# Optimization experiments

Hardware: AMD Instinct MI355X
Metric: run time of the kernel (lower is better)

Reference implementation:

```python
import jax, jax.numpy as jnp
import numpy as np

N_NODES = 100000
N_EDGES = 1600000
IN_DIM, HID_DIM, OUT_DIM = 32, 16, 8


def setup_inputs() -> dict:
    key = jax.random.key(0)
    ks = jax.random.split(key, 10)
    x = jax.random.normal(ks[0], (N_NODES, IN_DIM), dtype=jnp.float32)
    edge_index = jax.random.randint(ks[1], (2, N_EDGES), 0, N_NODES, dtype=jnp.int32)
    s1 = 1.0 / np.sqrt(IN_DIM)
    s2 = 1.0 / np.sqrt(HID_DIM)
    s3 = 1.0 / np.sqrt(OUT_DIM)
    return {
        "x": x,
        "edge_index": edge_index,
        # SAGEConv layer 1: lin_l (neighbor, with bias) and lin_r (root)
        "Wl1": jax.random.uniform(ks[2], (HID_DIM, IN_DIM), jnp.float32, -s1, s1),
        "bl1": jnp.zeros((HID_DIM,), jnp.float32),
        "Wr1": jax.random.uniform(ks[3], (HID_DIM, IN_DIM), jnp.float32, -s1, s1),
        # SAGEConv layer 2
        "Wl2": jax.random.uniform(ks[4], (OUT_DIM, HID_DIM), jnp.float32, -s2, s2),
        "bl2": jnp.zeros((OUT_DIM,), jnp.float32),
        "Wr2": jax.random.uniform(ks[5], (OUT_DIM, HID_DIM), jnp.float32, -s2, s2),
        # final Linear head
        "Wfc": jax.random.uniform(ks[6], (1, OUT_DIM), jnp.float32, -s3, s3),
        "bfc": jax.random.uniform(ks[7], (1,), jnp.float32, -s3, s3),
    }


def _sage_conv(x, src, dst, Wl, bl, Wr):
    # mean-aggregate neighbor messages x[src] at destination nodes
    msg_sum = jax.ops.segment_sum(x[src], dst, num_segments=N_NODES)  # [N, d]
    deg = jax.ops.segment_sum(jnp.ones((src.shape[0],), x.dtype), dst, num_segments=N_NODES)
    mean = msg_sum / jnp.maximum(deg, 1.0)[:, None]
    # out = lin_l(mean_neighbors) + lin_r(x_root)
    return mean @ Wl.T + bl + x @ Wr.T


def reference(x, edge_index, Wl1, bl1, Wr1, Wl2, bl2, Wr2, Wfc, bfc):
    src, dst = edge_index[0], edge_index[1]
    h = _sage_conv(x, src, dst, Wl1, bl1, Wr1)
    h = jax.nn.relu(h)
    h = _sage_conv(h, src, dst, Wl2, bl2, Wr2)
    return h @ Wfc.T + bfc  # [N, 1]
```

## Files before the change

### kernel.cpp

```cpp
#include <hip/hip_runtime.h>
#include <hip/hip_fp16.h>

#define NN 100000
#define NE 1600000
#define IN_DIM 32
#define HID_DIM 16
#define OUT_DIM 8

#define NPB 128
#define NBK ((NN + NPB - 1) / NPB)
#define CAP 3200
#define EPB 4096
#define EPT (EPB / 256)
#define NT_BUCKET ((NE + EPB - 1) / EPB)
#define NT_PRE1 ((NN + 255) / 256)
#define GRID1 (NT_BUCKET + NT_PRE1)
#define BF_STRIDE 16
#define SCAN_CHUNKS ((NBK + 255) / 256)

__global__ __launch_bounds__(256) void k_phase1(
    const float* __restrict__ x, const int* __restrict__ src, const int* __restrict__ dst,
    const float* __restrict__ Wl1, const float* __restrict__ bl1, const float* __restrict__ Wr1,
    const float* __restrict__ Wl2, const float* __restrict__ bl2, const float* __restrict__ Wr2,
    const float* __restrict__ Wfc, const float* __restrict__ bfc,
    int* __restrict__ bucketfill, unsigned int* __restrict__ bucket,
    __half* __restrict__ zh, float* __restrict__ rb, float* __restrict__ uvc)
{
    __shared__ int lcnt[NBK];
    __shared__ int lpos[NBK];
    __shared__ int lbase[NBK];
    __shared__ int lfill[NBK];
    __shared__ int sscan[256];
    __shared__ unsigned int ssorted[EPB];
    __shared__ unsigned short sbin[EPB];
    int tid = threadIdx.x;

    if (blockIdx.x < NT_BUCKET) {
        int e0 = blockIdx.x * EPB;
        int e1 = min(e0 + EPB, NE);
        int total = e1 - e0;

        for (int i = tid; i < NBK; i += 256) lcnt[i] = 0;
        __syncthreads();

        int myd[EPT];
#pragma unroll
        for (int k = 0; k < EPT; k++) {
            int e = e0 + k * 256 + tid;
            myd[k] = (e < e1) ? dst[e] : -1;
            if (myd[k] >= 0) atomicAdd(&lcnt[myd[k] >> 7], 1);
        }
        __syncthreads();

        int carry = 0;
        for (int ch = 0; ch < SCAN_CHUNKS; ch++) {
            int idx = ch * 256 + tid;
            int v = (idx < NBK) ? lcnt[idx] : 0;
            sscan[tid] = v;
            __syncthreads();
            for (int off = 1; off < 256; off <<= 1) {
                int t2 = (tid >= off) ? sscan[tid - off] : 0;
                __syncthreads();
                sscan[tid] += t2;
                __syncthreads();
            }
            if (idx < NBK) lpos[idx] = carry + sscan[tid] - v;
            carry += sscan[255];
            __syncthreads();
        }

        for (int i = tid; i < NBK; i += 256) {
            lbase[i] = (lcnt[i] > 0) ? atomicAdd(&bucketfill[i * BF_STRIDE], lcnt[i]) : 0;
            lfill[i] = lpos[i];
        }
        __syncthreads();

#pragma unroll
        for (int k = 0; k < EPT; k++) {
            if (myd[k] >= 0) {
                int e = e0 + k * 256 + tid;
                int s = src[e];
                int b = myd[k] >> 7;
                int p = atomicAdd(&lfill[b], 1);
                ssorted[p] = (unsigned)(myd[k] & (NPB - 1)) | ((unsigned)s << 7);
                sbin[p] = (unsigned short)b;
            }
        }
        __syncthreads();

        for (int i = tid; i < total; i += 256) {
            int b = sbin[i];
            bucket[(size_t)b * CAP + lbase[b] + (i - lpos[b])] = ssorted[i];
        }
    } else {
        int chunk = blockIdx.x - NT_BUCKET;
        float* sWl = (float*)ssorted;
        float* sWr = sWl + 512;
        float* sb  = (float*)sbin;
        for (int i = tid; i < HID_DIM * IN_DIM; i += 256) {
            sWl[i] = Wl1[i];
            sWr[i] = Wr1[i];
        }
        if (tid < HID_DIM) sb[tid] = bl1[tid];
        if (chunk == 0) {
            if (tid < HID_DIM) {
                float uu = 0.f, vv = 0.f;
#pragma unroll
                for (int o = 0; o < OUT_DIM; o++) {
                    uu += Wfc[o] * Wl2[o * HID_DIM + tid];
                    vv += Wfc[o] * Wr2[o * HID_DIM + tid];
                }
                uvc[tid] = uu;
                uvc[HID_DIM + tid] = vv;
            }
            if (tid == 0) {
                float c0 = bfc[0];
#pragma unroll
                for (int o = 0; o < OUT_DIM; o++) c0 += Wfc[o] * bl2[o];
                uvc[2 * HID_DIM] = c0;
            }
        }
        __syncthreads();
        int n = chunk * 256 + tid;
        if (n < NN) {
            float xv[IN_DIM];
            const float4* x4 = (const float4*)(x + (size_t)n * IN_DIM);
#pragma unroll
            for (int c = 0; c < 8; c++) {
                float4 b = x4[c];
                xv[c * 4 + 0] = b.x; xv[c * 4 + 1] = b.y;
                xv[c * 4 + 2] = b.z; xv[c * 4 + 3] = b.w;
            }
            float zo[HID_DIM], ro[HID_DIM];
#pragma unroll
            for (int o = 0; o < HID_DIM; o++) {
                float az = 0.f, ar = sb[o];
#pragma unroll
                for (int i = 0; i < IN_DIM; i++) {
                    az += sWl[o * IN_DIM + i] * xv[i];
                    ar += sWr[o * IN_DIM + i] * xv[i];
                }
                zo[o] = az; ro[o] = ar;
            }
            __half2 hh[8];
#pragma unroll
            for (int c = 0; c < 8; c++) hh[c] = __floats2half2_rn(zo[2 * c], zo[2 * c + 1]);
            float4* zh4 = (float4*)(zh + (size_t)n * HID_DIM);
            zh4[0] = *(float4*)&hh[0];
            zh4[1] = *(float4*)&hh[4];
            float4* r4 = (float4*)(rb + (size_t)n * HID_DIM);
#pragma unroll
            for (int c = 0; c < 4; c++) {
                r4[c] = make_float4(ro[c*4], ro[c*4+1], ro[c*4+2], ro[c*4+3]);
            }
        }
    }
}

__global__ __launch_bounds__(256) void k_sort_gather(
    const int* __restrict__ bucketfill, const unsigned int* __restrict__ bucket,
    const __half* __restrict__ zh, const float* __restrict__ rb, const float* __restrict__ uvc,
    int* __restrict__ deg, float* __restrict__ sv, float* __restrict__ tv)
{
    __shared__ int lcnt[NPB];
    __shared__ int lscan[NPB];
    __shared__ int lfill[NPB];
    __shared__ int ssrc[CAP];

    int b = blockIdx.x;
    int tid = threadIdx.x;
    int cntb = bucketfill[b * BF_STRIDE];
    const unsigned int* bk = bucket + (size_t)b * CAP;

    if (tid < NPB) lcnt[tid] = 0;
    __syncthreads();
    for (int i = tid; i < cntb; i += 256) atomicAdd(&lcnt[bk[i] & (NPB - 1)], 1);
    __syncthreads();
    if (tid < NPB) lscan[tid] = lcnt[tid];
    __syncthreads();
    for (int off = 1; off < NPB; off <<= 1) {
        int tvv = (tid >= off && tid < NPB) ? lscan[tid - off] : 0;
        __syncthreads();
        if (tid < NPB) lscan[tid] += tvv;
        __syncthreads();
    }
    if (tid < NPB) {
        lfill[tid] = lscan[tid] - lcnt[tid];
        int node = b * NPB + tid;
        if (node < NN) deg[node] = lcnt[tid];
    }
    __syncthreads();
    for (int i = tid; i < cntb; i += 256) {
        unsigned v = bk[i];
        int d = v & (NPB - 1);
        int p = atomicAdd(&lfill[d], 1);
        ssrc[p] = (int)(v >> 7);
    }
    __syncthreads();

    int c = tid & 3;
    int nl0 = tid >> 2;
    float4 u4 = ((const float4*)uvc)[c];
    float4 v4 = ((const float4*)uvc)[4 + c];
    const float2* z2p = (const float2*)zh;
#pragma unroll
    for (int pass = 0; pass < 2; pass++) {
        int nl = pass * 64 + nl0;
        int n2 = b * NPB + nl;
        if (n2 < NN) {
            int dg = lcnt[nl];
            int st = lscan[nl] - dg;
            float4 acc = {0.f, 0.f, 0.f, 0.f};
            int i = 0;
            for (; i + 4 <= dg; i += 4) {
                int s0 = ssrc[st + i + 0];
                int s1 = ssrc[st + i + 1];
                int s2 = ssrc[st + i + 2];
                int s3 = ssrc[st + i + 3];
                float2 w0 = z2p[s0 * 4 + c];
                float2 w1 = z2p[s1 * 4 + c];
                float2 w2 = z2p[s2 * 4 + c];
                float2 w3 = z2p[s3 * 4 + c];
                float2 a0 = __half22float2(*(__half2*)&w0.x), b0 = __half22float2(*(__half2*)&w0.y);
                float2 a1 = __half22float2(*(__half2*)&w1.x), b1 = __half22float2(*(__half2*)&w1.y);
                float2 a2 = __half22float2(*(__half2*)&w2.x), b2 = __half22float2(*(__half2*)&w2.y);
                float2 a3 = __half22float2(*(__half2*)&w3.x), b3 = __half22float2(*(__half2*)&w3.y);
                acc.x += a0.x + a1.x + a2.x + a3.x;
                acc.y += a0.y + a1.y + a2.y + a3.y;
                acc.z += b0.x + b1.x + b2.x + b3.x;
                acc.w += b0.y + b1.y + b2.y + b3.y;
            }
            for (; i < dg; i++) {
                float2 w = z2p[ssrc[st + i] * 4 + c];
                float2 a = __half22float2(*(__half2*)&w.x), bb = __half22float2(*(__half2*)&w.y);
                acc.x += a.x; acc.y += a.y; acc.z += bb.x; acc.w += bb.y;
            }
            float inv = 1.0f / fmaxf((float)dg, 1.0f);
            float4 r = ((const float4*)rb)[n2 * 4 + c];
            float h0 = fmaxf(acc.x * inv + r.x, 0.f);
            float h1 = fmaxf(acc.y * inv + r.y, 0.f);
            float h2 = fmaxf(acc.z * inv + r.z, 0.f);
            float h3 = fmaxf(acc.w * inv + r.w, 0.f);
            float ps = u4.x * h0 + u4.y * h1 + u4.z * h2 + u4.w * h3;
            float pt = v4.x * h0 + v4.y * h1 + v4.z * h2 + v4.w * h3;
            ps += __shfl_xor(ps, 1);
            ps += __shfl_xor(ps, 2);
            pt += __shfl_xor(pt, 1);
            pt += __shfl_xor(pt, 2);
            if (c == 0) { sv[n2] = ps; tv[n2] = pt; }
        }
    }
}

__global__ __launch_bounds__(256) void k_final(
    const int* __restrict__ bucketfill, const unsigned int* __restrict__ bucket,
    const int* __restrict__ deg, const float* __restrict__ sv, const float* __restrict__ tv,
    const float* __restrict__ uvc, float* __restrict__ out)
{
    __shared__ float lsum[NPB];
    int b = blockIdx.x;
    int tid = threadIdx.x;
    int cntb = bucketfill[b * BF_STRIDE];
    const unsigned int* bk = bucket + (size_t)b * CAP;

    if (tid < NPB) lsum[tid] = 0.f;
    __syncthreads();
    for (int i = tid; i < cntb; i += 256) {
        unsigned v = bk[i];
        int d = v & (NPB - 1);
        int s = (int)(v >> 7);
        atomicAdd(&lsum[d], sv[s]);
    }
    __syncthreads();
    if (tid < NPB) {
        int n = b * NPB + tid;
        if (n < NN) {
            float dg = (float)deg[n];
            out[n] = lsum[tid] / fmaxf(dg, 1.0f) + tv[n] + uvc[2 * HID_DIM];
        }
    }
}

extern "C" void kernel_launch(void* const* d_in, const int* in_sizes, int n_in,
                              void* d_out, int out_size, void* d_ws, size_t ws_size,
                              hipStream_t stream) {
    const float* x   = (const float*)d_in[0];
    const int*   ei  = (const int*)d_in[1];
    const float* Wl1 = (const float*)d_in[2];
    const float* bl1 = (const float*)d_in[3];
    const float* Wr1 = (const float*)d_in[4];
    const float* Wl2 = (const float*)d_in[5];
    const float* bl2 = (const float*)d_in[6];
    const float* Wr2 = (const float*)d_in[7];
    const float* Wfc = (const float*)d_in[8];
    const float* bfc = (const float*)d_in[9];
    float* out = (float*)d_out;

    const int* src = ei;
    const int* dst = ei + NE;

    int* bucketfill = (int*)d_ws;
    int* deg        = bucketfill + 12544;
    float* uvc      = (float*)(deg + NN);
    float* sv       = uvc + 40;
    float* tv       = sv + NN;
    unsigned int* bucket = (unsigned int*)(tv + NN);
    __half* zh      = (__half*)(bucket + (size_t)NBK * CAP);
    float* rb       = (float*)(zh + (size_t)NN * HID_DIM);

    hipMemsetAsync(bucketfill, 0, NBK * BF_STRIDE * sizeof(int), stream);

    k_phase1<<<GRID1, 256, 0, stream>>>(x, src, dst, Wl1, bl1, Wr1,
                                        Wl2, bl2, Wr2, Wfc, bfc,
                                        bucketfill, bucket, zh, rb, uvc);
    k_sort_gather<<<NBK, 256, 0, stream>>>(bucketfill, bucket, zh, rb, uvc, deg, sv, tv);
    k_final<<<NBK, 256, 0, stream>>>(bucketfill, bucket, deg, sv, tv, uvc, out);
}
```

Baseline: 152.2 us.

## Use wavefront shuffle scans and halve edges per bucketing block

Replaces the shared-memory Hillis-Steele scans, which need many block-wide barriers, with 64-lane shuffle scans plus a small per-wave sum combine, in both the bucketing kernel and the per-bucket sort kernel. The edges handled per bucketing block drop from 4096 to 2048, which doubles the number of bucketing blocks and shrinks their shared-memory footprint. To fit the smaller ssorted buffer, the weight staging in the precompute branch moves to other shared arrays. The extra blocks each repeat the full scan over all buckets and issue more global atomics on the bucket fill counters.

```diff
diff --git a/kernel.cpp b/kernel.cpp
--- a/kernel.cpp
+++ b/kernel.cpp
@@ -10,7 +10,7 @@
 #define NPB 128
 #define NBK ((NN + NPB - 1) / NPB)
 #define CAP 3200
-#define EPB 4096
+#define EPB 2048
 #define EPT (EPB / 256)
 #define NT_BUCKET ((NE + EPB - 1) / EPB)
 #define NT_PRE1 ((NN + 255) / 256)
@@ -30,7 +30,7 @@
     __shared__ int lpos[NBK];
     __shared__ int lbase[NBK];
     __shared__ int lfill[NBK];
-    __shared__ int sscan[256];
+    __shared__ int swsum[4];
     __shared__ unsigned int ssorted[EPB];
     __shared__ unsigned short sbin[EPB];
     int tid = threadIdx.x;
@@ -39,6 +39,8 @@
         int e0 = blockIdx.x * EPB;
         int e1 = min(e0 + EPB, NE);
         int total = e1 - e0;
+        int lane = tid & 63;
+        int w = tid >> 6;
 
         for (int i = tid; i < NBK; i += 256) lcnt[i] = 0;
         __syncthreads();
@@ -56,16 +58,18 @@
         for (int ch = 0; ch < SCAN_CHUNKS; ch++) {
             int idx = ch * 256 + tid;
             int v = (idx < NBK) ? lcnt[idx] : 0;
-            sscan[tid] = v;
+            int incl = v;
+#pragma unroll
+            for (int off = 1; off < 64; off <<= 1) {
+                int t = __shfl_up(incl, off);
+                if (lane >= off) incl += t;
+            }
+            if (lane == 63) swsum[w] = incl;
             __syncthreads();
-            for (int off = 1; off < 256; off <<= 1) {
-                int t2 = (tid >= off) ? sscan[tid - off] : 0;
-                __syncthreads();
-                sscan[tid] += t2;
-                __syncthreads();
-            }
-            if (idx < NBK) lpos[idx] = carry + sscan[tid] - v;
-            carry += sscan[255];
+            int pre = carry;
+            for (int ww = 0; ww < w; ww++) pre += swsum[ww];
+            if (idx < NBK) lpos[idx] = pre + incl - v;
+            carry += swsum[0] + swsum[1] + swsum[2] + swsum[3];
             __syncthreads();
         }
 
@@ -94,9 +98,9 @@
         }
     } else {
         int chunk = blockIdx.x - NT_BUCKET;
-        float* sWl = (float*)ssorted;
-        float* sWr = sWl + 512;
-        float* sb  = (float*)sbin;
+        float* sWl = (float*)lcnt;
+        float* sWr = (float*)lbase;
+        float* sb  = (float*)ssorted;
         for (int i = tid; i < HID_DIM * IN_DIM; i += 256) {
             sWl[i] = Wl1[i];
             sWr[i] = Wr1[i];
@@ -165,6 +169,7 @@
     __shared__ int lcnt[NPB];
     __shared__ int lscan[NPB];
     __shared__ int lfill[NPB];
+    __shared__ int wsum0;
     __shared__ int ssrc[CAP];
 
     int b = blockIdx.x;
@@ -176,18 +181,25 @@
     __syncthreads();
     for (int i = tid; i < cntb; i += 256) atomicAdd(&lcnt[bk[i] & (NPB - 1)], 1);
     __syncthreads();
-    if (tid < NPB) lscan[tid] = lcnt[tid];
-    __syncthreads();
-    for (int off = 1; off < NPB; off <<= 1) {
-        int tvv = (tid >= off && tid < NPB) ? lscan[tid - off] : 0;
-        __syncthreads();
-        if (tid < NPB) lscan[tid] += tvv;
-        __syncthreads();
-    }
-    if (tid < NPB) {
-        lfill[tid] = lscan[tid] - lcnt[tid];
-        int node = b * NPB + tid;
-        if (node < NN) deg[node] = lcnt[tid];
+
+    {
+        int lane = tid & 63;
+        int v = (tid < NPB) ? lcnt[tid] : 0;
+        int incl = v;
+#pragma unroll
+        for (int off = 1; off < 64; off <<= 1) {
+            int t = __shfl_up(incl, off);
+            if (lane >= off) incl += t;
+        }
+        if (tid == 63) wsum0 = incl;
+        __syncthreads();
+        if (tid >= 64 && tid < NPB) incl += wsum0;
+        if (tid < NPB) {
+            lscan[tid] = incl;
+            lfill[tid] = incl - v;
+            int node = b * NPB + tid;
+            if (node < NN) deg[node] = v;
+        }
     }
     __syncthreads();
     for (int i = tid; i < cntb; i += 256) {
```

After: 177.7 us. 16.7% more time.
